# Kernel optimization log

Measured on AMD Instinct MI355X. Metric: run time of the kernel, lower is better.

Reference implementation:

```python
import jax, jax.numpy as jnp
import numpy as np
from jax import lax

B = 32768
L = 200          # window_size
K = 5            # conv kernel
CIN = 6
FLAT = L - K + 1  # 196, conv1d valid output length (out channels = 1)


def setup_inputs() -> dict:
    key = jax.random.key(0)
    ks = jax.random.split(key, 9)
    s = lambda *sh: 1.0 / np.sqrt(sh[-1])
    x = jax.random.normal(ks[0], (B, CIN, L), dtype=jnp.float32)
    conv_w = jax.random.normal(ks[1], (1, CIN, K), dtype=jnp.float32) * (1.0 / np.sqrt(CIN * K))
    conv_b = jax.random.normal(ks[2], (1,), dtype=jnp.float32) * 0.1
    w1 = jax.random.normal(ks[3], (FLAT, 50), dtype=jnp.float32) * (1.0 / np.sqrt(FLAT))
    b1 = jax.random.normal(ks[4], (50,), dtype=jnp.float32) * 0.1
    w2 = jax.random.normal(ks[5], (50, 30), dtype=jnp.float32) * (1.0 / np.sqrt(50))
    b2 = jax.random.normal(ks[6], (30,), dtype=jnp.float32) * 0.1
    w3 = jax.random.normal(ks[7], (30, 15), dtype=jnp.float32) * (1.0 / np.sqrt(30))
    b3 = jax.random.normal(ks[8], (15,), dtype=jnp.float32) * 0.1
    return {"x": x, "conv_w": conv_w, "conv_b": conv_b, "w1": w1, "b1": b1,
            "w2": w2, "b2": b2, "w3": w3, "b3": b3}


def reference(x, conv_w, conv_b, w1, b1, w2, b2, w3, b3):
    # conv1d (valid): [B,6,200] -> [B,1,196]
    y = lax.conv_general_dilated(x, conv_w, window_strides=(1,), padding='VALID',
                                 dimension_numbers=('NCH', 'OIH', 'NCH'))
    y = y + conv_b[None, :, None]
    h = y.reshape(x.shape[0], -1)                       # [B,196]
    h = jax.nn.relu(h @ w1 + b1)                        # [B,50]
    h = jax.nn.relu(h @ w2 + b2)                        # [B,30]
    out = h @ w3 + b3                                   # [B,15]
    # Procrustes orthogonalization of the 3x3 block
    R = out[:, :9].reshape(-1, 3, 3)
    U, _, VT = jnp.linalg.svd(R)                        # batched 3x3 SVD
    det = jnp.linalg.det(jnp.matmul(U, VT))             # [B]
    scale = jnp.stack([jnp.ones_like(det), jnp.ones_like(det), det], axis=1)  # diag(1,1,det)
    R_norm = jnp.matmul(U, VT * scale[:, :, None])      # U @ S @ VT
    return jnp.concatenate([R_norm.reshape(-1, 9), out[:, 9:]], axis=1)
```

## Files before the change

kernel.cpp:

```cpp
#include <hip/hip_runtime.h>
#include <math.h>

#define BATCH 32768
#define LW    200
#define CIN   6
#define KSZ   5
#define FLAT  196
#define NH1   50
#define NH2   30
#define NOUT  15

__global__ __launch_bounds__(256) void conv_kernel(
    const float* __restrict__ x, const float* __restrict__ cw,
    const float* __restrict__ cb, float* __restrict__ co)
{
    int t = blockIdx.x * 256 + threadIdx.x;
    int b = t / 49;
    int q = t - b * 49;
    int i0 = q * 4;

    float w[CIN][KSZ];
#pragma unroll
    for (int c = 0; c < CIN; ++c)
#pragma unroll
        for (int k = 0; k < KSZ; ++k) w[c][k] = cw[c * KSZ + k];
    float bias = cb[0];

    float acc0 = bias, acc1 = bias, acc2 = bias, acc3 = bias;
    const float* xb = x + (long)b * (CIN * LW) + i0;
#pragma unroll
    for (int c = 0; c < CIN; ++c) {
        float4 lo = *(const float4*)(xb + c * LW);
        float4 hi = *(const float4*)(xb + c * LW + 4);
        float xf[8] = {lo.x, lo.y, lo.z, lo.w, hi.x, hi.y, hi.z, hi.w};
#pragma unroll
        for (int k = 0; k < KSZ; ++k) {
            acc0 = fmaf(xf[k + 0], w[c][k], acc0);
            acc1 = fmaf(xf[k + 1], w[c][k], acc1);
            acc2 = fmaf(xf[k + 2], w[c][k], acc2);
            acc3 = fmaf(xf[k + 3], w[c][k], acc3);
        }
    }
    *(float4*)(co + (long)b * FLAT + i0) = make_float4(acc0, acc1, acc2, acc3);
}

__global__ __launch_bounds__(64) void mlp_kernel(
    const float* __restrict__ co,
    const float* __restrict__ w1, const float* __restrict__ b1,
    const float* __restrict__ w2, const float* __restrict__ b2,
    const float* __restrict__ w3, const float* __restrict__ b3,
    float* __restrict__ out)
{
    int b = blockIdx.x * 64 + threadIdx.x;

    float h1[NH1];
#pragma unroll
    for (int j = 0; j < NH1; ++j) h1[j] = b1[j];

    const float4* c4p = (const float4*)(co + (size_t)b * FLAT);
    for (int k = 0; k < FLAT / 4; ++k) {
        float4 c4 = c4p[k];
        float cv[4] = {c4.x, c4.y, c4.z, c4.w};
#pragma unroll
        for (int r = 0; r < 4; ++r) {
            const float* row = w1 + (4 * k + r) * NH1;
            float c = cv[r];
#pragma unroll
            for (int j = 0; j < NH1; ++j) h1[j] = fmaf(c, row[j], h1[j]);
        }
    }
#pragma unroll
    for (int j = 0; j < NH1; ++j) h1[j] = fmaxf(h1[j], 0.f);

    float h2[NH2];
#pragma unroll
    for (int j = 0; j < NH2; ++j) h2[j] = b2[j];
#pragma unroll
    for (int k = 0; k < NH1; ++k) {
        float hk = h1[k];
        const float* row = w2 + k * NH2;
#pragma unroll
        for (int j = 0; j < NH2; ++j) h2[j] = fmaf(hk, row[j], h2[j]);
    }
#pragma unroll
    for (int j = 0; j < NH2; ++j) h2[j] = fmaxf(h2[j], 0.f);

    float o[NOUT];
#pragma unroll
    for (int j = 0; j < NOUT; ++j) o[j] = b3[j];
#pragma unroll
    for (int k = 0; k < NH2; ++k) {
        float hk = h2[k];
        const float* row = w3 + k * NOUT;
#pragma unroll
        for (int j = 0; j < NOUT; ++j) o[j] = fmaf(hk, row[j], o[j]);
    }

    {
        float r00 = o[0], r01 = o[1], r02 = o[2];
        float r10 = o[3], r11 = o[4], r12 = o[5];
        float r20 = o[6], r21 = o[7], r22 = o[8];

        float A[4][4], V[4][4];
        A[0][0] = r00 + r11 + r22;
        A[1][1] = r00 - r11 - r22;
        A[2][2] = r11 - r00 - r22;
        A[3][3] = r22 - r00 - r11;
        A[0][1] = A[1][0] = r21 - r12;
        A[0][2] = A[2][0] = r02 - r20;
        A[0][3] = A[3][0] = r10 - r01;
        A[1][2] = A[2][1] = r01 + r10;
        A[1][3] = A[3][1] = r02 + r20;
        A[2][3] = A[3][2] = r12 + r21;
#pragma unroll
        for (int i = 0; i < 4; ++i)
#pragma unroll
            for (int j = 0; j < 4; ++j) V[i][j] = (i == j) ? 1.f : 0.f;

        const int pr[6][2] = {{0,1},{0,2},{0,3},{1,2},{1,3},{2,3}};
        for (int sweep = 0; sweep < 7; ++sweep) {
#pragma unroll
            for (int pi = 0; pi < 6; ++pi) {
                const int p = pr[pi][0], q = pr[pi][1];
                float apq = A[p][q];
                if (fabsf(apq) > 1e-20f) {
                    float theta = (A[q][q] - A[p][p]) / (2.f * apq);
                    float t = copysignf(1.f, theta) / (fabsf(theta) + sqrtf(1.f + theta * theta));
                    float c = rsqrtf(1.f + t * t);
                    float s = t * c;
#pragma unroll
                    for (int k = 0; k < 4; ++k) {
                        float akp = A[k][p], akq = A[k][q];
                        A[k][p] = c * akp - s * akq;
                        A[k][q] = s * akp + c * akq;
                    }
#pragma unroll
                    for (int k = 0; k < 4; ++k) {
                        float apk = A[p][k], aqk = A[q][k];
                        A[p][k] = c * apk - s * aqk;
                        A[q][k] = s * apk + c * aqk;
                    }
#pragma unroll
                    for (int k = 0; k < 4; ++k) {
                        float vkp = V[k][p], vkq = V[k][q];
                        V[k][p] = c * vkp - s * vkq;
                        V[k][q] = s * vkp + c * vkq;
                    }
                }
            }
        }

        int best = 0;
        float bl = A[0][0];
#pragma unroll
        for (int i = 1; i < 4; ++i)
            if (A[i][i] > bl) { bl = A[i][i]; best = i; }

        float vw = V[0][best], vx = V[1][best], vy = V[2][best], vz = V[3][best];
        float inv = rsqrtf(vw * vw + vx * vx + vy * vy + vz * vz);
        vw *= inv; vx *= inv; vy *= inv; vz *= inv;

        float xx = vx * vx, yy = vy * vy, zz = vz * vz;
        float xy = vx * vy, xz = vx * vz, yz = vy * vz;
        float wx = vw * vx, wy = vw * vy, wz = vw * vz;

        float* ob = out + (long)b * NOUT;
        ob[0]  = 1.f - 2.f * (yy + zz);
        ob[1]  = 2.f * (xy - wz);
        ob[2]  = 2.f * (xz + wy);
        ob[3]  = 2.f * (xy + wz);
        ob[4]  = 1.f - 2.f * (xx + zz);
        ob[5]  = 2.f * (yz - wx);
        ob[6]  = 2.f * (xz - wy);
        ob[7]  = 2.f * (yz + wx);
        ob[8]  = 1.f - 2.f * (xx + yy);
        ob[9]  = o[9];
        ob[10] = o[10];
        ob[11] = o[11];
        ob[12] = o[12];
        ob[13] = o[13];
        ob[14] = o[14];
    }
}

extern "C" void kernel_launch(void* const* d_in, const int* in_sizes, int n_in,
                              void* d_out, int out_size, void* d_ws, size_t ws_size,
                              hipStream_t stream) {
    const float* x  = (const float*)d_in[0];
    const float* cw = (const float*)d_in[1];
    const float* cb = (const float*)d_in[2];
    const float* w1 = (const float*)d_in[3];
    const float* b1 = (const float*)d_in[4];
    const float* w2 = (const float*)d_in[5];
    const float* b2 = (const float*)d_in[6];
    const float* w3 = (const float*)d_in[7];
    const float* b3 = (const float*)d_in[8];
    float* outp = (float*)d_out;
    float* co   = (float*)d_ws;

    conv_kernel<<<(BATCH * 49) / 256, 256, 0, stream>>>(x, cw, cb, co);
    mlp_kernel<<<BATCH / 64, 64, 0, stream>>>(co, w1, b1, w2, b2, w3, b3, outp);
}
```

Before: 331.5 us.

## Fuse conv into MLP kernel with split-K across four waves

```diff
diff --git a/kernel.cpp b/kernel.cpp
--- a/kernel.cpp
+++ b/kernel.cpp
@@ -10,67 +10,92 @@
 #define NH2   30
 #define NOUT  15
 
-__global__ __launch_bounds__(256) void conv_kernel(
-    const float* __restrict__ x, const float* __restrict__ cw,
-    const float* __restrict__ cb, float* __restrict__ co)
-{
-    int t = blockIdx.x * 256 + threadIdx.x;
-    int b = t / 49;
-    int q = t - b * 49;
-    int i0 = q * 4;
-
-    float w[CIN][KSZ];
-#pragma unroll
-    for (int c = 0; c < CIN; ++c)
-#pragma unroll
-        for (int k = 0; k < KSZ; ++k) w[c][k] = cw[c * KSZ + k];
-    float bias = cb[0];
-
-    float acc0 = bias, acc1 = bias, acc2 = bias, acc3 = bias;
-    const float* xb = x + (long)b * (CIN * LW) + i0;
-#pragma unroll
-    for (int c = 0; c < CIN; ++c) {
-        float4 lo = *(const float4*)(xb + c * LW);
-        float4 hi = *(const float4*)(xb + c * LW + 4);
-        float xf[8] = {lo.x, lo.y, lo.z, lo.w, hi.x, hi.y, hi.z, hi.w};
-#pragma unroll
-        for (int k = 0; k < KSZ; ++k) {
-            acc0 = fmaf(xf[k + 0], w[c][k], acc0);
-            acc1 = fmaf(xf[k + 1], w[c][k], acc1);
-            acc2 = fmaf(xf[k + 2], w[c][k], acc2);
-            acc3 = fmaf(xf[k + 3], w[c][k], acc3);
-        }
-    }
-    *(float4*)(co + (long)b * FLAT + i0) = make_float4(acc0, acc1, acc2, acc3);
-}
-
-__global__ __launch_bounds__(64) void mlp_kernel(
-    const float* __restrict__ co,
+__global__ __launch_bounds__(256) void fused_kernel(
+    const float* __restrict__ x,
+    const float* __restrict__ cw, const float* __restrict__ cb,
     const float* __restrict__ w1, const float* __restrict__ b1,
     const float* __restrict__ w2, const float* __restrict__ b2,
     const float* __restrict__ w3, const float* __restrict__ b3,
     float* __restrict__ out)
 {
-    int b = blockIdx.x * 64 + threadIdx.x;
+    __shared__ float part[3][64][53];
+
+    const int tid  = threadIdx.x;
+    const int wv   = __builtin_amdgcn_readfirstlane(tid >> 6);
+    const int lane = tid & 63;
+    const int b    = blockIdx.x * 64 + lane;
+
+    const int KST[4] = {0, 52, 100, 148};
+    const int kstart = KST[wv];
+    const int nchunk = (wv == 0) ? 13 : 12;
+
+    float w[CIN][KSZ];
+#pragma unroll
+    for (int c = 0; c < CIN; ++c)
+#pragma unroll
+        for (int k = 0; k < KSZ; ++k) w[c][k] = cw[c * KSZ + k];
+    const float bias = cb[0];
+
+    float h1p[NH1];
+#pragma unroll
+    for (int j = 0; j < NH1; ++j) h1p[j] = 0.f;
+
+    const float* xb = x + (size_t)b * (CIN * LW) + kstart;
+    float4 cur[CIN], nxt[CIN];
+#pragma unroll
+    for (int c = 0; c < CIN; ++c) {
+        cur[c] = *(const float4*)(xb + c * LW);
+        nxt[c] = *(const float4*)(xb + c * LW + 4);
+    }
+
+    for (int c = 0; c < nchunk; ++c) {
+        int pf = c + 2; if (pf > nchunk) pf = nchunk;
+        float4 fut[CIN];
+#pragma unroll
+        for (int ch = 0; ch < CIN; ++ch)
+            fut[ch] = *(const float4*)(xb + ch * LW + 4 * pf);
+
+        float a0 = bias, a1 = bias, a2 = bias, a3 = bias;
+#pragma unroll
+        for (int ch = 0; ch < CIN; ++ch) {
+            float xf[8] = {cur[ch].x, cur[ch].y, cur[ch].z, cur[ch].w,
+                           nxt[ch].x, nxt[ch].y, nxt[ch].z, nxt[ch].w};
+#pragma unroll
+            for (int k = 0; k < KSZ; ++k) {
+                a0 = fmaf(xf[k + 0], w[ch][k], a0);
+                a1 = fmaf(xf[k + 1], w[ch][k], a1);
+                a2 = fmaf(xf[k + 2], w[ch][k], a2);
+                a3 = fmaf(xf[k + 3], w[ch][k], a3);
+            }
+        }
+
+        const float* wrow = w1 + (size_t)(kstart + 4 * c) * NH1;
+#pragma unroll
+        for (int j = 0; j < NH1; ++j) h1p[j] = fmaf(a0, wrow[j], h1p[j]);
+#pragma unroll
+        for (int j = 0; j < NH1; ++j) h1p[j] = fmaf(a1, wrow[NH1 + j], h1p[j]);
+#pragma unroll
+        for (int j = 0; j < NH1; ++j) h1p[j] = fmaf(a2, wrow[2 * NH1 + j], h1p[j]);
+#pragma unroll
+        for (int j = 0; j < NH1; ++j) h1p[j] = fmaf(a3, wrow[3 * NH1 + j], h1p[j]);
+
+#pragma unroll
+        for (int ch = 0; ch < CIN; ++ch) { cur[ch] = nxt[ch]; nxt[ch] = fut[ch]; }
+    }
+
+    if (wv != 0) {
+#pragma unroll
+        for (int j = 0; j < NH1; ++j) part[wv - 1][lane][j] = h1p[j];
+    }
+    __syncthreads();
+    if (wv != 0) return;
 
     float h1[NH1];
 #pragma unroll
-    for (int j = 0; j < NH1; ++j) h1[j] = b1[j];
-
-    const float4* c4p = (const float4*)(co + (size_t)b * FLAT);
-    for (int k = 0; k < FLAT / 4; ++k) {
-        float4 c4 = c4p[k];
-        float cv[4] = {c4.x, c4.y, c4.z, c4.w};
-#pragma unroll
-        for (int r = 0; r < 4; ++r) {
-            const float* row = w1 + (4 * k + r) * NH1;
-            float c = cv[r];
-#pragma unroll
-            for (int j = 0; j < NH1; ++j) h1[j] = fmaf(c, row[j], h1[j]);
-        }
-    }
-#pragma unroll
-    for (int j = 0; j < NH1; ++j) h1[j] = fmaxf(h1[j], 0.f);
+    for (int j = 0; j < NH1; ++j) {
+        float s = h1p[j] + part[0][lane][j] + part[1][lane][j] + part[2][lane][j] + b1[j];
+        h1[j] = fmaxf(s, 0.f);
+    }
 
     float h2[NH2];
 #pragma unroll
@@ -196,8 +221,6 @@
     const float* w3 = (const float*)d_in[7];
     const float* b3 = (const float*)d_in[8];
     float* outp = (float*)d_out;
-    float* co   = (float*)d_ws;
-
-    conv_kernel<<<(BATCH * 49) / 256, 256, 0, stream>>>(x, cw, cb, co);
-    mlp_kernel<<<BATCH / 64, 64, 0, stream>>>(co, w1, b1, w2, b2, w3, b3, outp);
+
+    fused_kernel<<<BATCH / 64, 256, 0, stream>>>(x, cw, cb, w1, b1, w2, b2, w3, b3, outp);
 }
```

After: 556.1 us. 1.68x slower.
